# Kernel optimization log

Measured on AMD Instinct MI355X. Metric: run time of the kernel, lower is better.

## Reference

```python
import jax, jax.numpy as jnp
import numpy as np

B, N, DIN, DH = 16, 512, 128, 256
NEG = -9.0e15  # matches -9000000000000000.0 in torch source


def _xavier(key, fan_in, fan_out):
    lim = float(np.sqrt(6.0 / (fan_in + fan_out)))
    return jax.random.uniform(key, (fan_in, fan_out), jnp.float32, -lim, lim)


def _l2n(x, eps=1e-12):
    # torch F.normalize: x / max(||x||, eps)
    return x / jnp.maximum(jnp.linalg.norm(x, axis=-1, keepdims=True), eps)


def _prelu(x, a):
    return jnp.where(x >= 0, x, a * x)


def setup_inputs() -> dict:
    key = jax.random.key(0)
    ks = jax.random.split(key, 12)
    seq = jax.random.normal(ks[0], (B, N, DIN), jnp.float32)
    # sparse-ish nonnegative adjacency with self loops, row-normalized
    u = jax.random.uniform(ks[1], (B, N, N), jnp.float32)
    a = jnp.where(u < 0.1, u, 0.0) + jnp.eye(N, dtype=jnp.float32)[None]
    adj = a / a.sum(-1, keepdims=True)
    # dense diffusion matrix, row-normalized
    d = jax.random.uniform(ks[2], (B, N, N), jnp.float32)
    diff = d / d.sum(-1, keepdims=True)
    # dropout keep-mask for F.dropout(p=0.1, training=True)
    keep = jax.random.bernoulli(ks[3], 0.9, (B, N, N)).astype(jnp.float32)
    drop_mask = keep / 0.9
    return {
        "seq": seq, "adj": adj, "diff": diff, "drop_mask": drop_mask,
        "fc1_w": _xavier(ks[4], DIN, DH),
        "q_w": _xavier(ks[5], DH, DH),
        "k_w": _xavier(ks[6], DH, DH),
        "v_w1": _xavier(ks[7], DH, DH),
        "v_w2": _xavier(ks[8], DH, DH),
        "fc2_w": _xavier(ks[9], DIN, DH),
        "bias1": jnp.zeros((DH,), jnp.float32),
        "bias2": jnp.zeros((DH,), jnp.float32),
        "prelu1_a": jnp.float32(0.25),
        "prelu2_a": jnp.float32(0.25),
        "v_prelu_a": jnp.float32(0.25),
    }


def reference(seq, adj, diff, drop_mask, fc1_w, q_w, k_w, v_w1, v_w2,
              fc2_w, bias1, bias2, prelu1_a, prelu2_a, v_prelu_a):
    # ---- GCN1 (attention branch) ----
    fts = seq @ fc1_w                                   # [B,N,H]
    out = jnp.einsum('bmn,bnh->bmh', adj, fts)          # adj aggregation
    q = _l2n(out @ q_w)
    k = _l2n(out @ k_w)
    scores = jax.lax.stop_gradient(jnp.einsum('bmd,bnd->bmn', q, k))  # .detach()
    div_loss = jnp.mean(jnp.sum((q - k) ** 2, axis=-1))
    att = jnp.where(adj > 0, scores, NEG)
    att = jax.nn.softmax(att, axis=-1) * drop_mask      # dropout(p=0.1)
    agg = jnp.einsum('bmn,bnh->bmh', att, out)
    v = _prelu(agg @ v_w1, v_prelu_a) @ v_w2 + bias1
    h1 = _prelu(v, prelu1_a)
    # ---- GCN2 (plain branch) ----
    h2 = _prelu(jnp.einsum('bmn,bnh->bmh', diff, seq @ fc2_w) + bias2, prelu2_a)
    # ---- Readout ----
    c1 = jnp.mean(h1, axis=1)                           # [B,H]
    c2 = jnp.mean(h2, axis=1)
    # ---- DIS ----
    n1 = _l2n(h1).reshape(B * N, DH)
    n2 = _l2n(h2).reshape(B * N, DH)
    node_logits = n1 @ n2.T                             # [B*N, B*N]
    graph_logits = _l2n(c1) @ _l2n(c2).T                # [B, B]
    return node_logits, graph_logits, div_loss
```

## Files before the change

### kernel.cpp

```cpp
#include <hip/hip_runtime.h>
#include <hip/hip_bf16.h>


using bf16x8 = __attribute__((ext_vector_type(8))) short;
using f32x4  = __attribute__((ext_vector_type(4))) float;

__device__ __forceinline__ unsigned short f2b(float f) {
    union { float f; unsigned int u; } x; x.f = f;
    unsigned int r = x.u + 0x7FFFu + ((x.u >> 16) & 1u);
    return (unsigned short)(r >> 16);
}
__device__ __forceinline__ void gload_lds16(const void* g, void* l) {
    __builtin_amdgcn_global_load_lds(
        (const __attribute__((address_space(1))) void*)g,
        (__attribute__((address_space(3))) void*)l, 16, 0, 0);
}

__global__ __launch_bounds__(256) void prep(
    const float* __restrict__ seq, const float* __restrict__ adj,
    const float* __restrict__ diff,
    const float* __restrict__ fc1, const float* __restrict__ fc2,
    const float* __restrict__ qw,  const float* __restrict__ kw,
    const float* __restrict__ v1,  const float* __restrict__ v2,
    unsigned short* __restrict__ seq_bf, unsigned short* __restrict__ adj_bf,
    unsigned short* __restrict__ diff_bf,
    unsigned short* fc1T, unsigned short* fc2T, unsigned short* qwT,
    unsigned short* kwT,  unsigned short* v1T,  unsigned short* v2T)
{
    __shared__ float t[32][33];
    const int bid = blockIdx.x, tid = threadIdx.x;
    if (bid < 9216) {
        long i = (long)bid * 256 + tid;
        const float* src; unsigned short* dst; long off;
        if (i < 262144)       { src = seq;  dst = seq_bf;  off = i; }
        else if (i < 1310720) { src = adj;  dst = adj_bf;  off = i - 262144; }
        else                  { src = diff; dst = diff_bf; off = i - 1310720; }
        float4 v = reinterpret_cast<const float4*>(src)[off];
        ushort4 o; o.x = f2b(v.x); o.y = f2b(v.y); o.z = f2b(v.z); o.w = f2b(v.w);
        reinterpret_cast<ushort4*>(dst)[off] = o;
        return;
    }
    const int r = bid - 9216;
    const int z = r >> 6;
    const float* in; unsigned short* op; int R;
    if      (z == 0) { in = fc1; op = fc1T; R = 128; }
    else if (z == 1) { in = fc2; op = fc2T; R = 128; }
    else if (z == 2) { in = qw;  op = qwT;  R = 256; }
    else if (z == 3) { in = kw;  op = kwT;  R = 256; }
    else if (z == 4) { in = v1;  op = v1T;  R = 256; }
    else             { in = v2;  op = v2T;  R = 256; }
    const int c0 = (r & 7) * 32, r0 = ((r >> 3) & 7) * 32;
    if (r0 >= R) return;
    const int x = tid & 31, y = tid >> 5;
    for (int i = 0; i < 32; i += 8) t[y + i][x] = in[(long)(r0 + y + i) * 256 + c0 + x];
    __syncthreads();
    for (int i = 0; i < 32; i += 8)
        op[(long)(c0 + y + i) * R + r0 + x] = f2b(t[x][y + i]);
}

#define BN 128
#define BK 64

template<int TBM, bool WF, bool WB, bool SWZ>
__global__ __launch_bounds__(256) void gemm_nt(
    const unsigned short* __restrict__ A, const unsigned short* __restrict__ Bt,
    float* __restrict__ Cf, unsigned short* __restrict__ Cb,
    int M, int Nn, int K, int lda, int ldb, int ldc,
    long sA, long sB, long sC)
{
    constexpr int MI = TBM / 32;
    __shared__ unsigned short As[TBM][BK];
    __shared__ unsigned short Bs[BN][BK];
    const int b = blockIdx.z;
    A  += (long)b * sA;
    Bt += (long)b * sB;
    const long cbase = (long)b * sC;

    int tx, ty;
    if (SWZ) {
        int bid = blockIdx.y * gridDim.x + blockIdx.x;
        int nwg = gridDim.x * gridDim.y;
        int cpx = nwg >> 3;
        int s = (bid & 7) * cpx + (bid >> 3);
        tx = s % gridDim.x; ty = s / gridDim.x;
    } else { tx = blockIdx.x; ty = blockIdx.y; }
    const int tile_m = ty * TBM;
    const int tile_n = tx * BN;

    const int tid  = threadIdx.x;
    const int lane = tid & 63;
    const int wave = tid >> 6;
    const int wm = (wave >> 1) * (TBM / 2);
    const int wn = (wave & 1) << 6;
    const int lrow = lane >> 3;
    const int lcol = (lane & 7) << 3;

    f32x4 acc[MI][4] = {};

    for (int k0 = 0; k0 < K; k0 += BK) {
        #pragma unroll
        for (int i = 0; i < TBM / 32; ++i) {
            const int rb = (i * 4 + wave) * 8;
            gload_lds16(A + (long)(tile_m + rb + lrow) * lda + k0 + lcol, &As[rb][0]);
        }
        #pragma unroll
        for (int i = 0; i < 4; ++i) {
            const int rb = (i * 4 + wave) * 8;
            gload_lds16(Bt + (long)(tile_n + rb + lrow) * ldb + k0 + lcol, &Bs[rb][0]);
        }
        __syncthreads();
        #pragma unroll
        for (int ks = 0; ks < 2; ++ks) {
            const int kk = ks * 32 + ((lane >> 4) << 3);
            bf16x8 af[MI], bq[4];
            #pragma unroll
            for (int mi = 0; mi < MI; ++mi)
                af[mi] = *reinterpret_cast<const bf16x8*>(&As[wm + (lane & 15) + mi * 16][kk]);
            #pragma unroll
            for (int ni = 0; ni < 4; ++ni)
                bq[ni] = *reinterpret_cast<const bf16x8*>(&Bs[wn + (lane & 15) + ni * 16][kk]);
            #pragma unroll
            for (int mi = 0; mi < MI; ++mi)
                #pragma unroll
                for (int ni = 0; ni < 4; ++ni)
                    acc[mi][ni] = __builtin_amdgcn_mfma_f32_16x16x32_bf16(
                        af[mi], bq[ni], acc[mi][ni], 0, 0, 0);
        }
        __syncthreads();
    }

    const int c0 = lane & 15;
    const int r0 = (lane >> 4) << 2;
    #pragma unroll
    for (int ni = 0; ni < 4; ++ni) {
        const int col = tile_n + wn + ni * 16 + c0;
        #pragma unroll
        for (int mi = 0; mi < MI; ++mi) {
            const int row0 = tile_m + wm + mi * 16 + r0;
            if (WF) {
                #pragma unroll
                for (int j = 0; j < 4; ++j)
                    __builtin_nontemporal_store(acc[mi][ni][j],
                        &Cf[cbase + (long)(row0 + j) * ldc + col]);
            }
            if (WB) {
                #pragma unroll
                for (int j = 0; j < 4; ++j)
                    Cb[cbase + (long)(row0 + j) * ldc + col] = f2b(acc[mi][ni][j]);
            }
        }
    }
}

__global__ __launch_bounds__(256) void gcn1qk(
    const unsigned short* __restrict__ adj_bf,
    const unsigned short* __restrict__ ftsT,
    const unsigned short* __restrict__ qkT,
    unsigned short* __restrict__ outT,
    unsigned short* __restrict__ q_bf,
    unsigned short* __restrict__ k_bf)
{
    __shared__ unsigned char smem[86528];
    unsigned short* Ot  = (unsigned short*)smem;
    unsigned short* As  = (unsigned short*)(smem + 16896);
    unsigned short* Bs  = (unsigned short*)(smem + 20992);
    unsigned short* Bs2 = (unsigned short*)(smem + 20992);
    __shared__ float sred[32][4];

    const int b  = blockIdx.y;
    const int m0 = blockIdx.x << 5;
    const unsigned short* ap = adj_bf + ((long)b * 512 + m0) * 512;

    const int tid = threadIdx.x, lane = tid & 63, wave = tid >> 6;
    const int lrow = lane >> 3, lcol = (lane & 7) << 3;
    const int hi = lane >> 4, c0 = lane & 15, r0 = hi << 2;

    {
        const int wn = wave << 6;
        f32x4 acc[2][4] = {};
        for (int k0 = 0; k0 < 512; k0 += 64) {
            gload_lds16(ap + (long)(wave * 8 + lrow) * 512 + k0 + lcol, &As[wave * 8 * 64]);
            #pragma unroll
            for (int i = 0; i < 8; ++i) {
                const int rb = (i * 4 + wave) * 8;
                gload_lds16(ftsT + (long)(rb + lrow) * 8192 + b * 512 + k0 + lcol, &Bs[rb * 64]);
            }
            __syncthreads();
            #pragma unroll
            for (int ks = 0; ks < 2; ++ks) {
                const int kk = ks * 32 + (hi << 3);
                bf16x8 af[2], bq[4];
                #pragma unroll
                for (int mi = 0; mi < 2; ++mi)
                    af[mi] = *reinterpret_cast<const bf16x8*>(&As[(mi * 16 + c0) * 64 + kk]);
                #pragma unroll
                for (int ni = 0; ni < 4; ++ni)
                    bq[ni] = *reinterpret_cast<const bf16x8*>(&Bs[(wn + ni * 16 + c0) * 64 + kk]);
                #pragma unroll
                for (int mi = 0; mi < 2; ++mi)
                    #pragma unroll
                    for (int ni = 0; ni < 4; ++ni)
                        acc[mi][ni] = __builtin_amdgcn_mfma_f32_16x16x32_bf16(
                            af[mi], bq[ni], acc[mi][ni], 0, 0, 0);
            }
            __syncthreads();
        }
        #pragma unroll
        for (int mi = 0; mi < 2; ++mi)
            #pragma unroll
            for (int ni = 0; ni < 4; ++ni) {
                const int col = wn + ni * 16 + c0;
                ushort4 o;
                unsigned short* e = (unsigned short*)&o;
                #pragma unroll
                for (int j = 0; j < 4; ++j) {
                    unsigned short v = f2b(acc[mi][ni][j]);
                    e[j] = v;
                    Ot[(mi * 16 + r0 + j) * 264 + col] = v;
                }
                *reinterpret_cast<ushort4*>(
                    &outT[(long)b * 131072 + (long)col * 512 + m0 + mi * 16 + r0]) = o;
            }
    }
    __syncthreads();

    {
        const int wn = wave << 7;
        f32x4 acc[2][8] = {};
        for (int k0 = 0; k0 < 256; k0 += 64) {
            #pragma unroll
            for (int i = 0; i < 16; ++i) {
                const int rb = (i * 4 + wave) * 8;
                gload_lds16(qkT + (long)(rb + lrow) * 256 + k0 + lcol, &Bs2[rb * 64]);
            }
            __syncthreads();
            #pragma unroll
            for (int ks = 0; ks < 2; ++ks) {
                const int kk = ks * 32 + (hi << 3);
                bf16x8 af[2], bq[8];
                #pragma unroll
                for (int mi = 0; mi < 2; ++mi)
                    af[mi] = *reinterpret_cast<const bf16x8*>(&Ot[(mi * 16 + c0) * 264 + k0 + kk]);
                #pragma unroll
                for (int ni = 0; ni < 8; ++ni)
                    bq[ni] = *reinterpret_cast<const bf16x8*>(&Bs2[(wn + ni * 16 + c0) * 64 + kk]);
                #pragma unroll
                for (int mi = 0; mi < 2; ++mi)
                    #pragma unroll
                    for (int ni = 0; ni < 8; ++ni)
                        acc[mi][ni] = __builtin_amdgcn_mfma_f32_16x16x32_bf16(
                            af[mi], bq[ni], acc[mi][ni], 0, 0, 0);
            }
            __syncthreads();
        }
        float rs[2][4] = {};
        #pragma unroll
        for (int mi = 0; mi < 2; ++mi)
            #pragma unroll
            for (int ni = 0; ni < 8; ++ni)
                #pragma unroll
                for (int j = 0; j < 4; ++j) { float x = acc[mi][ni][j]; rs[mi][j] += x * x; }
        #pragma unroll
        for (int o = 1; o <= 8; o <<= 1)
            #pragma unroll
            for (int mi = 0; mi < 2; ++mi)
                #pragma unroll
                for (int j = 0; j < 4; ++j) rs[mi][j] += __shfl_xor(rs[mi][j], o);
        if (c0 == 0) {
            #pragma unroll
            for (int mi = 0; mi < 2; ++mi)
                #pragma unroll
                for (int j = 0; j < 4; ++j) sred[mi * 16 + r0 + j][wave] = rs[mi][j];
        }
        __syncthreads();
        float inv[2][4];
        #pragma unroll
        for (int mi = 0; mi < 2; ++mi)
            #pragma unroll
            for (int j = 0; j < 4; ++j) {
                const int rr = mi * 16 + r0 + j;
                float sq = sred[rr][0] + sred[rr][1];
                float sk = sred[rr][2] + sred[rr][3];
                inv[mi][j] = 1.f / fmaxf(sqrtf(wave < 2 ? sq : sk), 1e-12f);
            }
        #pragma unroll
        for (int mi = 0; mi < 2; ++mi)
            #pragma unroll
            for (int ni = 0; ni < 8; ++ni)
                #pragma unroll
                for (int j = 0; j < 4; ++j) {
                    const long rowg = (long)b * 512 + m0 + mi * 16 + r0 + j;
                    const int col = wn + ni * 16 + c0;
                    unsigned short v = f2b(acc[mi][ni][j] * inv[mi][j]);
                    if (wave < 2) q_bf[rowg * 256 + col] = v;
                    else          k_bf[rowg * 256 + col - 256] = v;
                }
    }
}

__global__ __launch_bounds__(256) void attmlp(
    const unsigned short* __restrict__ q_bf,
    const unsigned short* __restrict__ k_bf,
    const unsigned short* __restrict__ adj_bf,
    const float* __restrict__ drop,
    const unsigned short* __restrict__ outT,
    const unsigned short* __restrict__ w1T,
    const unsigned short* __restrict__ w2T,
    const float* __restrict__ bias,
    const float* __restrict__ av, const float* __restrict__ a1,
    unsigned short* __restrict__ n_out,
    float* __restrict__ psum,
    float* __restrict__ rowpart)
{
    __shared__ unsigned char smem[69632];
    unsigned short* As  = (unsigned short*)smem;
    unsigned short* Bs  = (unsigned short*)(smem + 4096);
    unsigned short* Pls = (unsigned short*)smem;
    unsigned short* Bs2 = (unsigned short*)(smem + 34816);
    unsigned short* T   = (unsigned short*)smem;
    unsigned short* Bs3 = (unsigned short*)(smem + 16896);
    __shared__ float redm[32][4], reds[32][4];

    const int b  = blockIdx.y;
    const int m0 = blockIdx.x << 5;
    const unsigned short* qp = q_bf + (long)b * 131072 + (long)m0 * 256;
    const unsigned short* kp = k_bf + (long)b * 131072;
    const unsigned short* ot = outT + (long)b * 131072;
    const unsigned short* ap = adj_bf + ((long)b * 512 + m0) * 512;
    const float*          dp = drop   + ((long)b * 512 + m0) * 512;

    const int tid = threadIdx.x, lane = tid & 63, wave = tid >> 6;
    const int lrow = lane >> 3, lcol = (lane & 7) << 3;
    const int hi = lane >> 4, c0 = lane & 15, r0 = hi << 2;

    {
        const int wn = wave << 7;
        f32x4 acc[2][8] = {};
        for (int k0 = 0; k0 < 256; k0 += 64) {
            gload_lds16(qp + (long)(wave * 8 + lrow) * 256 + k0 + lcol, &As[wave * 8 * 64]);
            #pragma unroll
            for (int i = 0; i < 16; ++i) {
                const int rb = (i * 4 + wave) * 8;
                gload_lds16(kp + (long)(rb + lrow) * 256 + k0 + lcol, &Bs[rb * 64]);
            }
            __syncthreads();
            #pragma unroll
            for (int ks = 0; ks < 2; ++ks) {
                const int kk = ks * 32 + (hi << 3);
                bf16x8 af[2], bq[8];
                #pragma unroll
                for (int mi = 0; mi < 2; ++mi)
                    af[mi] = *reinterpret_cast<const bf16x8*>(&As[(mi * 16 + c0) * 64 + kk]);
                #pragma unroll
                for (int ni = 0; ni < 8; ++ni)
                    bq[ni] = *reinterpret_cast<const bf16x8*>(&Bs[(wn + ni * 16 + c0) * 64 + kk]);
                #pragma unroll
                for (int mi = 0; mi < 2; ++mi)
                    #pragma unroll
                    for (int ni = 0; ni < 8; ++ni)
                        acc[mi][ni] = __builtin_amdgcn_mfma_f32_16x16x32_bf16(
                            af[mi], bq[ni], acc[mi][ni], 0, 0, 0);
            }
            __syncthreads();
        }

        float rmax[2][4];
        #pragma unroll
        for (int mi = 0; mi < 2; ++mi)
            #pragma unroll
            for (int j = 0; j < 4; ++j) rmax[mi][j] = -3.0e38f;
        #pragma unroll
        for (int mi = 0; mi < 2; ++mi)
            #pragma unroll
            for (int ni = 0; ni < 8; ++ni)
                #pragma unroll
                for (int j = 0; j < 4; ++j) {
                    const int rowl = mi * 16 + r0 + j;
                    const int col  = wn + ni * 16 + c0;
                    float s = acc[mi][ni][j];
                    if (col == m0 + rowl)
                        rowpart[(long)b * 512 + m0 + rowl] = 2.f - 2.f * s;
                    bool m = ap[(long)rowl * 512 + col] != 0;
                    s = m ? s : -3.0e38f;
                    acc[mi][ni][j] = s;
                    rmax[mi][j] = fmaxf(rmax[mi][j], s);
                }
        #pragma unroll
        for (int o = 1; o <= 8; o <<= 1)
            #pragma unroll
            for (int mi = 0; mi < 2; ++mi)
                #pragma unroll
                for (int j = 0; j < 4; ++j)
                    rmax[mi][j] = fmaxf(rmax[mi][j], __shfl_xor(rmax[mi][j], o));
        if (c0 == 0) {
            #pragma unroll
            for (int mi = 0; mi < 2; ++mi)
                #pragma unroll
                for (int j = 0; j < 4; ++j) redm[mi * 16 + r0 + j][wave] = rmax[mi][j];
        }
        __syncthreads();
        float mx[2][4], rsum[2][4];
        #pragma unroll
        for (int mi = 0; mi < 2; ++mi)
            #pragma unroll
            for (int j = 0; j < 4; ++j) {
                const int rr = mi * 16 + r0 + j;
                mx[mi][j] = fmaxf(fmaxf(redm[rr][0], redm[rr][1]), fmaxf(redm[rr][2], redm[rr][3]));
                rsum[mi][j] = 0.f;
            }
        #pragma unroll
        for (int mi = 0; mi < 2; ++mi)
            #pragma unroll
            for (int ni = 0; ni < 8; ++ni)
                #pragma unroll
                for (int j = 0; j < 4; ++j) {
                    float e = __expf(acc[mi][ni][j] - mx[mi][j]);
                    acc[mi][ni][j] = e;
                    rsum[mi][j] += e;
                }
        #pragma unroll
        for (int o = 1; o <= 8; o <<= 1)
            #pragma unroll
            for (int mi = 0; mi < 2; ++mi)
                #pragma unroll
                for (int j = 0; j < 4; ++j) rsum[mi][j] += __shfl_xor(rsum[mi][j], o);
        if (c0 == 0) {
            #pragma unroll
            for (int mi = 0; mi < 2; ++mi)
                #pragma unroll
                for (int j = 0; j < 4; ++j) reds[mi * 16 + r0 + j][wave] = rsum[mi][j];
        }
        __syncthreads();
        float inv[2][4];
        #pragma unroll
        for (int mi = 0; mi < 2; ++mi)
            #pragma unroll
            for (int j = 0; j < 4; ++j) {
                const int rr = mi * 16 + r0 + j;
                inv[mi][j] = 1.f / (reds[rr][0] + reds[rr][1] + reds[rr][2] + reds[rr][3]);
            }
        #pragma unroll
        for (int mi = 0; mi < 2; ++mi)
            #pragma unroll
            for (int ni = 0; ni < 8; ++ni)
                #pragma unroll
                for (int j = 0; j < 4; ++j) {
                    const int rowl = mi * 16 + r0 + j;
                    const int col  = wn + ni * 16 + c0;
                    float p = acc[mi][ni][j] * inv[mi][j] * dp[(long)rowl * 512 + col];
                    Pls[rowl * 520 + col] = f2b(p);
                }
    }
    __syncthreads();

    f32x4 acc2[2][4] = {};
    {
        const int wn = wave << 6;
        for (int k0 = 0; k0 < 512; k0 += 64) {
            #pragma unroll
            for (int i = 0; i < 8; ++i) {
                const int rb = (i * 4 + wave) * 8;
                gload_lds16(ot + (long)(rb + lrow) * 512 + k0 + lcol, &Bs2[rb * 64]);
            }
            __syncthreads();
            #pragma unroll
            for (int ks = 0; ks < 2; ++ks) {
                const int kk = ks * 32 + (hi << 3);
                bf16x8 af[2], bq[4];
                #pragma unroll
                for (int mi = 0; mi < 2; ++mi)
                    af[mi] = *reinterpret_cast<const bf16x8*>(&Pls[(mi * 16 + c0) * 520 + k0 + kk]);
                #pragma unroll
                for (int ni = 0; ni < 4; ++ni)
                    bq[ni] = *reinterpret_cast<const bf16x8*>(&Bs2[(wn + ni * 16 + c0) * 64 + kk]);
                #pragma unroll
                for (int mi = 0; mi < 2; ++mi)
                    #pragma unroll
                    for (int ni = 0; ni < 4; ++ni)
                        acc2[mi][ni] = __builtin_amdgcn_mfma_f32_16x16x32_bf16(
                            af[mi], bq[ni], acc2[mi][ni], 0, 0, 0);
            }
            __syncthreads();
        }
    }

    const int wn6 = wave << 6;
    const float alphav = av[0];
    #pragma unroll
    for (int mi = 0; mi < 2; ++mi)
        #pragma unroll
        for (int ni = 0; ni < 4; ++ni)
            #pragma unroll
            for (int j = 0; j < 4; ++j)
                T[(mi * 16 + r0 + j) * 264 + wn6 + ni * 16 + c0] = f2b(acc2[mi][ni][j]);
    f32x4 acct[2][4] = {};
    for (int k0 = 0; k0 < 256; k0 += 64) {
        #pragma unroll
        for (int i = 0; i < 8; ++i) {
            const int rb = (i * 4 + wave) * 8;
            gload_lds16(w1T + (long)(rb + lrow) * 256 + k0 + lcol, &Bs3[rb * 64]);
        }
        __syncthreads();
        #pragma unroll
        for (int ks = 0; ks < 2; ++ks) {
            const int kk = ks * 32 + (hi << 3);
            bf16x8 af[2], bq[4];
            #pragma unroll
            for (int mi = 0; mi < 2; ++mi)
                af[mi] = *reinterpret_cast<const bf16x8*>(&T[(mi * 16 + c0) * 264 + k0 + kk]);
            #pragma unroll
            for (int ni = 0; ni < 4; ++ni)
                bq[ni] = *reinterpret_cast<const bf16x8*>(&Bs3[(wn6 + ni * 16 + c0) * 64 + kk]);
            #pragma unroll
            for (int mi = 0; mi < 2; ++mi)
                #pragma unroll
                for (int ni = 0; ni < 4; ++ni)
                    acct[mi][ni] = __builtin_amdgcn_mfma_f32_16x16x32_bf16(
                        af[mi], bq[ni], acct[mi][ni], 0, 0, 0);
        }
        __syncthreads();
    }
    #pragma unroll
    for (int mi = 0; mi < 2; ++mi)
        #pragma unroll
        for (int ni = 0; ni < 4; ++ni)
            #pragma unroll
            for (int j = 0; j < 4; ++j) {
                float x = acct[mi][ni][j];
                x = (x >= 0.f) ? x : alphav * x;
                T[(mi * 16 + r0 + j) * 264 + wn6 + ni * 16 + c0] = f2b(x);
            }

    f32x4 acc3[2][4] = {};
    for (int k0 = 0; k0 < 256; k0 += 64) {
        #pragma unroll
        for (int i = 0; i < 8; ++i) {
            const int rb = (i * 4 + wave) * 8;
            gload_lds16(w2T + (long)(rb + lrow) * 256 + k0 + lcol, &Bs3[rb * 64]);
        }
        __syncthreads();
        #pragma unroll
        for (int ks = 0; ks < 2; ++ks) {
            const int kk = ks * 32 + (hi << 3);
            bf16x8 af[2], bq[4];
            #pragma unroll
            for (int mi = 0; mi < 2; ++mi)
                af[mi] = *reinterpret_cast<const bf16x8*>(&T[(mi * 16 + c0) * 264 + k0 + kk]);
            #pragma unroll
            for (int ni = 0; ni < 4; ++ni)
                bq[ni] = *reinterpret_cast<const bf16x8*>(&Bs3[(wn6 + ni * 16 + c0) * 64 + kk]);
            #pragma unroll
            for (int mi = 0; mi < 2; ++mi)
                #pragma unroll
                for (int ni = 0; ni < 4; ++ni)
                    acc3[mi][ni] = __builtin_amdgcn_mfma_f32_16x16x32_bf16(
                        af[mi], bq[ni], acc3[mi][ni], 0, 0, 0);
        }
        __syncthreads();
    }

    const float alpha1 = a1[0];
    float rs[2][4] = {};
    #pragma unroll
    for (int ni = 0; ni < 4; ++ni) {
        const float bv = bias[wn6 + ni * 16 + c0];
        #pragma unroll
        for (int mi = 0; mi < 2; ++mi)
            #pragma unroll
            for (int j = 0; j < 4; ++j) {
                float x = acc3[mi][ni][j] + bv;
                x = (x >= 0.f) ? x : alpha1 * x;
                acc3[mi][ni][j] = x;
                rs[mi][j] += x * x;
            }
    }
    #pragma unroll
    for (int o = 1; o <= 8; o <<= 1)
        #pragma unroll
        for (int mi = 0; mi < 2; ++mi)
            #pragma unroll
            for (int j = 0; j < 4; ++j) rs[mi][j] += __shfl_xor(rs[mi][j], o);
    if (c0 == 0) {
        #pragma unroll
        for (int mi = 0; mi < 2; ++mi)
            #pragma unroll
            for (int j = 0; j < 4; ++j) redm[mi * 16 + r0 + j][wave] = rs[mi][j];
    }
    __syncthreads();
    float inv2[2][4];
    #pragma unroll
    for (int mi = 0; mi < 2; ++mi)
        #pragma unroll
        for (int j = 0; j < 4; ++j) {
            const int rr = mi * 16 + r0 + j;
            float s = redm[rr][0] + redm[rr][1] + redm[rr][2] + redm[rr][3];
            inv2[mi][j] = 1.f / fmaxf(sqrtf(s), 1e-12f);
        }
    float cs[4];
    #pragma unroll
    for (int ni = 0; ni < 4; ++ni) {
        float s = 0.f;
        #pragma unroll
        for (int mi = 0; mi < 2; ++mi)
            #pragma unroll
            for (int j = 0; j < 4; ++j) s += acc3[mi][ni][j];
        s += __shfl_xor(s, 16);
        s += __shfl_xor(s, 32);
        cs[ni] = s;
    }
    const int p = b * 16 + blockIdx.x;
    if (lane < 16) {
        #pragma unroll
        for (int ni = 0; ni < 4; ++ni)
            psum[(long)p * 256 + wn6 + ni * 16 + lane] = cs[ni];
    }
    const long row0g = (long)b * 512 + m0;
    #pragma unroll
    for (int mi = 0; mi < 2; ++mi)
        #pragma unroll
        for (int ni = 0; ni < 4; ++ni)
            #pragma unroll
            for (int j = 0; j < 4; ++j)
                n_out[(row0g + mi * 16 + r0 + j) * 256 + wn6 + ni * 16 + c0] =
                    f2b(acc3[mi][ni][j] * inv2[mi][j]);
}

__global__ __launch_bounds__(256) void gemm_norm(
    const unsigned short* __restrict__ A, const unsigned short* __restrict__ Bt,
    unsigned short* __restrict__ n_out, float* __restrict__ psum,
    const float* __restrict__ bias, const float* __restrict__ alpha_ptr,
    int K, int lda, int ldb, long sA, long sB)
{
    __shared__ unsigned short As[32][BK];
    __shared__ unsigned short Bs[256][BK];
    __shared__ float rowred[32][4];
    A  += (long)blockIdx.z * sA;
    Bt += (long)blockIdx.z * sB;
    const int p = blockIdx.z * gridDim.y + blockIdx.y;
    const int arow0 = blockIdx.y * 32;
    const long grow0 = (long)p * 32;

    const int tid  = threadIdx.x;
    const int lane = tid & 63;
    const int wave = tid >> 6;
    const int wn = wave << 6;
    const int lrow = lane >> 3;
    const int lcol = (lane & 7) << 3;

    f32x4 acc[2][4] = {};

    for (int k0 = 0; k0 < K; k0 += BK) {
        {
            const int rb = wave * 8;
            gload_lds16(A + (long)(arow0 + rb + lrow) * lda + k0 + lcol, &As[rb][0]);
        }
        #pragma unroll
        for (int i = 0; i < 8; ++i) {
            const int rb = (i * 4 + wave) * 8;
            gload_lds16(Bt + (long)(rb + lrow) * ldb + k0 + lcol, &Bs[rb][0]);
        }
        __syncthreads();
        #pragma unroll
        for (int ks = 0; ks < 2; ++ks) {
            const int kk = ks * 32 + ((lane >> 4) << 3);
            bf16x8 af[2], bq[4];
            #pragma unroll
            for (int mi = 0; mi < 2; ++mi)
                af[mi] = *reinterpret_cast<const bf16x8*>(&As[(lane & 15) + mi * 16][kk]);
            #pragma unroll
            for (int ni = 0; ni < 4; ++ni)
                bq[ni] = *reinterpret_cast<const bf16x8*>(&Bs[wn + (lane & 15) + ni * 16][kk]);
            #pragma unroll
            for (int mi = 0; mi < 2; ++mi)
                #pragma unroll
                for (int ni = 0; ni < 4; ++ni)
                    acc[mi][ni] = __builtin_amdgcn_mfma_f32_16x16x32_bf16(
                        af[mi], bq[ni], acc[mi][ni], 0, 0, 0);
        }
        __syncthreads();
    }

    const float alpha = alpha_ptr[0];
    const int c0 = lane & 15;
    const int r0 = (lane >> 4) << 2;
    float rs[2][4] = {};
    #pragma unroll
    for (int ni = 0; ni < 4; ++ni) {
        const float bv = bias[wn + ni * 16 + c0];
        #pragma unroll
        for (int mi = 0; mi < 2; ++mi)
            #pragma unroll
            for (int j = 0; j < 4; ++j) {
                float x = acc[mi][ni][j] + bv;
                x = (x >= 0.f) ? x : alpha * x;
                acc[mi][ni][j] = x;
                rs[mi][j] += x * x;
            }
    }
    #pragma unroll
    for (int o = 1; o <= 8; o <<= 1)
        #pragma unroll
        for (int mi = 0; mi < 2; ++mi)
            #pragma unroll
            for (int j = 0; j < 4; ++j) rs[mi][j] += __shfl_xor(rs[mi][j], o);
    if ((lane & 15) == 0) {
        #pragma unroll
        for (int mi = 0; mi < 2; ++mi)
            #pragma unroll
            for (int j = 0; j < 4; ++j) rowred[mi * 16 + r0 + j][wave] = rs[mi][j];
    }
    __syncthreads();
    float inv[2][4];
    #pragma unroll
    for (int mi = 0; mi < 2; ++mi)
        #pragma unroll
        for (int j = 0; j < 4; ++j) {
            const int r = mi * 16 + r0 + j;
            float s = rowred[r][0] + rowred[r][1] + rowred[r][2] + rowred[r][3];
            inv[mi][j] = 1.f / fmaxf(sqrtf(s), 1e-12f);
        }
    float cs[4];
    #pragma unroll
    for (int ni = 0; ni < 4; ++ni) {
        float s = 0.f;
        #pragma unroll
        for (int mi = 0; mi < 2; ++mi)
            #pragma unroll
            for (int j = 0; j < 4; ++j) s += acc[mi][ni][j];
        s += __shfl_xor(s, 16);
        s += __shfl_xor(s, 32);
        cs[ni] = s;
    }
    if (lane < 16) {
        #pragma unroll
        for (int ni = 0; ni < 4; ++ni)
            psum[(long)p * 256 + wn + ni * 16 + lane] = cs[ni];
    }
    #pragma unroll
    for (int ni = 0; ni < 4; ++ni)
        #pragma unroll
        for (int mi = 0; mi < 2; ++mi)
            #pragma unroll
            for (int j = 0; j < 4; ++j)
                n_out[(grow0 + mi * 16 + r0 + j) * 256 + wn + ni * 16 + c0] =
                    f2b(acc[mi][ni][j] * inv[mi][j]);
}

__global__ __launch_bounds__(256) void creduce(const float* __restrict__ psum1,
                                               const float* __restrict__ psum2,
                                               float* __restrict__ c1n,
                                               float* __restrict__ c2n) {
    const int which = blockIdx.x & 1, g = blockIdx.x >> 1;
    const float* ps = which ? psum2 : psum1;
    float* cn = which ? c2n : c1n;
    const int t = threadIdx.x;
    float s = 0.f;
    #pragma unroll
    for (int c = 0; c < 16; ++c) s += ps[(long)(g * 16 + c) * 256 + t];
    s *= (1.f / 512.f);
    float ss = s * s;
    #pragma unroll
    for (int o = 32; o; o >>= 1) ss += __shfl_xor(ss, o);
    __shared__ float red[4];
    if ((t & 63) == 0) red[t >> 6] = ss;
    __syncthreads();
    float tot = red[0] + red[1] + red[2] + red[3];
    cn[g * 256 + t] = s / fmaxf(sqrtf(tot), 1e-12f);
}

__global__ __launch_bounds__(256) void graphf3(const float* __restrict__ c1n,
                                               const float* __restrict__ c2n,
                                               const float* __restrict__ rowpart,
                                               float* __restrict__ out_g,
                                               float* __restrict__ out_div) {
    const int t = threadIdx.x, ii = t >> 4, jj = t & 15;
    float s = 0.f;
    for (int h = 0; h < 256; ++h) s += c1n[ii * 256 + h] * c2n[jj * 256 + h];
    out_g[ii * 16 + jj] = s;
    float ds = 0.f;
    for (int i = t; i < 8192; i += 256) ds += rowpart[i];
    #pragma unroll
    for (int o = 32; o; o >>= 1) ds += __shfl_xor(ds, o);
    __shared__ float red[4];
    if ((t & 63) == 0) red[t >> 6] = ds;
    __syncthreads();
    if (t == 0) out_div[0] = (red[0] + red[1] + red[2] + red[3]) * (1.f / 8192.f);
}

static constexpr long OFF_SEQ_BF  = 0;
static constexpr long OFF_FC1T    = 2097152;
static constexpr long OFF_QWT     = 2228224;
static constexpr long OFF_VW1T    = 2490368;
static constexpr long OFF_VW2T    = 2621440;
static constexpr long OFF_ADJ     = 3145728;
static constexpr long OFF_DIFF    = 11534336;
static constexpr long OFF_FTST    = 19922944;
static constexpr long OFF_OUTT    = 28311552;
static constexpr long OFF_QBF     = 32505856;
static constexpr long OFF_KBF     = 36700160;
static constexpr long OFF_N1      = 40894464;
static constexpr long OFF_N2      = 45088768;
static constexpr long OFF_PSUM    = 49283072;
static constexpr long OFF_ROWPART = 49807360;
static constexpr long OFF_C1N     = 49840128;
static constexpr long OFF_C2N     = 49856512;

extern "C" void kernel_launch(void* const* d_in, const int* in_sizes, int n_in,
                              void* d_out, int out_size, void* d_ws, size_t ws_size,
                              hipStream_t stream) {
    const float* seq      = (const float*)d_in[0];
    const float* adj      = (const float*)d_in[1];
    const float* diff     = (const float*)d_in[2];
    const float* drop     = (const float*)d_in[3];
    const float* fc1_w    = (const float*)d_in[4];
    const float* q_w      = (const float*)d_in[5];
    const float* k_w      = (const float*)d_in[6];
    const float* v_w1     = (const float*)d_in[7];
    const float* v_w2     = (const float*)d_in[8];
    const float* fc2_w    = (const float*)d_in[9];
    const float* bias1    = (const float*)d_in[10];
    const float* bias2    = (const float*)d_in[11];
    const float* prelu1_a = (const float*)d_in[12];
    const float* prelu2_a = (const float*)d_in[13];
    const float* v_prelu  = (const float*)d_in[14];
    float* out = (float*)d_out;

    char* ws = (char*)d_ws;
    unsigned short* seq_bf  = (unsigned short*)(ws + OFF_SEQ_BF);
    unsigned short* fc1T    = (unsigned short*)(ws + OFF_FC1T);
    unsigned short* fc2T    = (unsigned short*)(ws + OFF_FC1T + 65536);
    unsigned short* qwT     = (unsigned short*)(ws + OFF_QWT);
    unsigned short* kwT     = (unsigned short*)(ws + OFF_QWT + 131072);
    unsigned short* vw1T    = (unsigned short*)(ws + OFF_VW1T);
    unsigned short* vw2T    = (unsigned short*)(ws + OFF_VW2T);
    unsigned short* adj_bf  = (unsigned short*)(ws + OFF_ADJ);
    unsigned short* diff_bf = (unsigned short*)(ws + OFF_DIFF);
    unsigned short* ftsT    = (unsigned short*)(ws + OFF_FTST);
    unsigned short* fts2T   = (unsigned short*)(ws + OFF_FTST + 4194304);
    unsigned short* outT    = (unsigned short*)(ws + OFF_OUTT);
    unsigned short* q_bf    = (unsigned short*)(ws + OFF_QBF);
    unsigned short* k_bf    = (unsigned short*)(ws + OFF_KBF);
    unsigned short* n1_bf   = (unsigned short*)(ws + OFF_N1);
    unsigned short* n2_bf   = (unsigned short*)(ws + OFF_N2);
    float*          psum1   = (float*)(ws + OFF_PSUM);
    float*          psum2   = (float*)(ws + OFF_PSUM + 262144);
    float*          rowpart = (float*)(ws + OFF_ROWPART);
    float*          c1n     = (float*)(ws + OFF_C1N);
    float*          c2n     = (float*)(ws + OFF_C2N);

    prep<<<9600, 256, 0, stream>>>(seq, adj, diff, fc1_w, fc2_w, q_w, k_w, v_w1, v_w2,
                                   seq_bf, adj_bf, diff_bf, fc1T, fc2T, qwT, kwT, vw1T, vw2T);

    gemm_nt<64, false, true, false><<<dim3(64, 4, 2), 256, 0, stream>>>(
        fc1T, seq_bf, nullptr, ftsT,
        256, 8192, 128, 128, 128, 8192, 32768, 0, 2097152);

    gcn1qk<<<dim3(16, 16), 256, 0, stream>>>(adj_bf, ftsT, qwT, outT, q_bf, k_bf);

    gemm_norm<<<dim3(1, 16, 16), 256, 0, stream>>>(
        diff_bf, fts2T, n2_bf, psum2, bias2, prelu2_a, 512, 512, 8192, 262144, 512);

    attmlp<<<dim3(16, 16), 256, 0, stream>>>(
        q_bf, k_bf, adj_bf, drop, outT, vw1T, vw2T, bias1, v_prelu, prelu1_a,
        n1_bf, psum1, rowpart);

    creduce<<<32, 256, 0, stream>>>(psum1, psum2, c1n, c2n);
    graphf3<<<1, 256, 0, stream>>>(c1n, c2n, rowpart, out + 67108864, out + 67109120);

    gemm_nt<128, true, false, true><<<dim3(64, 64, 1), 256, 0, stream>>>(
        n1_bf, n2_bf, out, nullptr,
        8192, 8192, 256, 256, 256, 8192, 0, 0, 0);

    (void)in_sizes; (void)n_in; (void)out_size; (void)ws_size;
}
```

Measured before the change: 212.5 us.

## Halve gcn1qk row tile and merge GCN2 norm kernel into attention kernel

gcn1qk now processes 16 rows per block instead of 32, doubling the grid to 512 blocks and shrinking shared memory so more blocks can run per CU. The separate GCN2 gemm_norm launch is folded into the attention/MLP kernel: odd blocks run the attention path and even blocks run the diffusion GEMM with bias, PReLU and normalization, so the two independent branches share one launch and fill the device together. The large node-logits store also switches from nontemporal to regular stores. The trade-offs are lower MFMA reuse per block in gcn1qk and possible load imbalance between the two block types in the merged kernel.

```diff
diff --git a/kernel.cpp b/kernel.cpp
--- a/kernel.cpp
+++ b/kernel.cpp
@@ -140,8 +140,7 @@
             if (WF) {
                 #pragma unroll
                 for (int j = 0; j < 4; ++j)
-                    __builtin_nontemporal_store(acc[mi][ni][j],
-                        &Cf[cbase + (long)(row0 + j) * ldc + col]);
+                    Cf[cbase + (long)(row0 + j) * ldc + col] = acc[mi][ni][j];
             }
             if (WB) {
                 #pragma unroll
@@ -160,15 +159,15 @@
     unsigned short* __restrict__ q_bf,
     unsigned short* __restrict__ k_bf)
 {
-    __shared__ unsigned char smem[86528];
+    __shared__ unsigned char smem[73984];
     unsigned short* Ot  = (unsigned short*)smem;
-    unsigned short* As  = (unsigned short*)(smem + 16896);
-    unsigned short* Bs  = (unsigned short*)(smem + 20992);
-    unsigned short* Bs2 = (unsigned short*)(smem + 20992);
-    __shared__ float sred[32][4];
+    unsigned short* As  = (unsigned short*)(smem + 8448);
+    unsigned short* Bs  = (unsigned short*)(smem + 10496);
+    unsigned short* Bs2 = (unsigned short*)(smem + 8448);
+    __shared__ float sred[16][4];
 
     const int b  = blockIdx.y;
-    const int m0 = blockIdx.x << 5;
+    const int m0 = blockIdx.x << 4;
     const unsigned short* ap = adj_bf + ((long)b * 512 + m0) * 512;
 
     const int tid = threadIdx.x, lane = tid & 63, wave = tid >> 6;
@@ -177,9 +176,10 @@
 
     {
         const int wn = wave << 6;
-        f32x4 acc[2][4] = {};
+        f32x4 acc[4] = {};
         for (int k0 = 0; k0 < 512; k0 += 64) {
-            gload_lds16(ap + (long)(wave * 8 + lrow) * 512 + k0 + lcol, &As[wave * 8 * 64]);
+            if (wave < 2)
+                gload_lds16(ap + (long)(wave * 8 + lrow) * 512 + k0 + lcol, &As[wave * 8 * 64]);
             #pragma unroll
             for (int i = 0; i < 8; ++i) {
                 const int rb = (i * 4 + wave) * 8;
@@ -189,44 +189,34 @@
             #pragma unroll
             for (int ks = 0; ks < 2; ++ks) {
                 const int kk = ks * 32 + (hi << 3);
-                bf16x8 af[2], bq[4];
-                #pragma unroll
-                for (int mi = 0; mi < 2; ++mi)
-                    af[mi] = *reinterpret_cast<const bf16x8*>(&As[(mi * 16 + c0) * 64 + kk]);
-                #pragma unroll
-                for (int ni = 0; ni < 4; ++ni)
-                    bq[ni] = *reinterpret_cast<const bf16x8*>(&Bs[(wn + ni * 16 + c0) * 64 + kk]);
-                #pragma unroll
-                for (int mi = 0; mi < 2; ++mi)
-                    #pragma unroll
-                    for (int ni = 0; ni < 4; ++ni)
-                        acc[mi][ni] = __builtin_amdgcn_mfma_f32_16x16x32_bf16(
-                            af[mi], bq[ni], acc[mi][ni], 0, 0, 0);
-            }
-            __syncthreads();
-        }
-        #pragma unroll
-        for (int mi = 0; mi < 2; ++mi)
-            #pragma unroll
-            for (int ni = 0; ni < 4; ++ni) {
-                const int col = wn + ni * 16 + c0;
-                ushort4 o;
-                unsigned short* e = (unsigned short*)&o;
-                #pragma unroll
-                for (int j = 0; j < 4; ++j) {
-                    unsigned short v = f2b(acc[mi][ni][j]);
-                    e[j] = v;
-                    Ot[(mi * 16 + r0 + j) * 264 + col] = v;
-                }
-                *reinterpret_cast<ushort4*>(
-                    &outT[(long)b * 131072 + (long)col * 512 + m0 + mi * 16 + r0]) = o;
-            }
+                bf16x8 af = *reinterpret_cast<const bf16x8*>(&As[c0 * 64 + kk]);
+                #pragma unroll
+                for (int ni = 0; ni < 4; ++ni) {
+                    bf16x8 bq = *reinterpret_cast<const bf16x8*>(&Bs[(wn + ni * 16 + c0) * 64 + kk]);
+                    acc[ni] = __builtin_amdgcn_mfma_f32_16x16x32_bf16(af, bq, acc[ni], 0, 0, 0);
+                }
+            }
+            __syncthreads();
+        }
+        #pragma unroll
+        for (int ni = 0; ni < 4; ++ni) {
+            const int col = wn + ni * 16 + c0;
+            ushort4 o;
+            unsigned short* e = (unsigned short*)&o;
+            #pragma unroll
+            for (int j = 0; j < 4; ++j) {
+                unsigned short v = f2b(acc[ni][j]);
+                e[j] = v;
+                Ot[(r0 + j) * 264 + col] = v;
+            }
+            *reinterpret_cast<ushort4*>(
+                &outT[(long)b * 131072 + (long)col * 512 + m0 + r0]) = o;
+        }
     }
-    __syncthreads();
 
     {
         const int wn = wave << 7;
-        f32x4 acc[2][8] = {};
+        f32x4 acc[8] = {};
         for (int k0 = 0; k0 < 256; k0 += 64) {
             #pragma unroll
             for (int i = 0; i < 16; ++i) {
@@ -237,68 +227,51 @@
             #pragma unroll
             for (int ks = 0; ks < 2; ++ks) {
                 const int kk = ks * 32 + (hi << 3);
-                bf16x8 af[2], bq[8];
-                #pragma unroll
-                for (int mi = 0; mi < 2; ++mi)
-                    af[mi] = *reinterpret_cast<const bf16x8*>(&Ot[(mi * 16 + c0) * 264 + k0 + kk]);
-                #pragma unroll
-                for (int ni = 0; ni < 8; ++ni)
-                    bq[ni] = *reinterpret_cast<const bf16x8*>(&Bs2[(wn + ni * 16 + c0) * 64 + kk]);
-                #pragma unroll
-                for (int mi = 0; mi < 2; ++mi)
-                    #pragma unroll
-                    for (int ni = 0; ni < 8; ++ni)
-                        acc[mi][ni] = __builtin_amdgcn_mfma_f32_16x16x32_bf16(
-                            af[mi], bq[ni], acc[mi][ni], 0, 0, 0);
-            }
-            __syncthreads();
-        }
-        float rs[2][4] = {};
-        #pragma unroll
-        for (int mi = 0; mi < 2; ++mi)
-            #pragma unroll
-            for (int ni = 0; ni < 8; ++ni)
-                #pragma unroll
-                for (int j = 0; j < 4; ++j) { float x = acc[mi][ni][j]; rs[mi][j] += x * x; }
+                bf16x8 af = *reinterpret_cast<const bf16x8*>(&Ot[c0 * 264 + k0 + kk]);
+                #pragma unroll
+                for (int ni = 0; ni < 8; ++ni) {
+                    bf16x8 bq = *reinterpret_cast<const bf16x8*>(&Bs2[(wn + ni * 16 + c0) * 64 + kk]);
+                    acc[ni] = __builtin_amdgcn_mfma_f32_16x16x32_bf16(af, bq, acc[ni], 0, 0, 0);
+                }
+            }
+            __syncthreads();
+        }
+        float rs[4] = {};
+        #pragma unroll
+        for (int ni = 0; ni < 8; ++ni)
+            #pragma unroll
+            for (int j = 0; j < 4; ++j) { float x = acc[ni][j]; rs[j] += x * x; }
         #pragma unroll
         for (int o = 1; o <= 8; o <<= 1)
             #pragma unroll
-            for (int mi = 0; mi < 2; ++mi)
-                #pragma unroll
-                for (int j = 0; j < 4; ++j) rs[mi][j] += __shfl_xor(rs[mi][j], o);
+            for (int j = 0; j < 4; ++j) rs[j] += __shfl_xor(rs[j], o);
         if (c0 == 0) {
             #pragma unroll
-            for (int mi = 0; mi < 2; ++mi)
-                #pragma unroll
-                for (int j = 0; j < 4; ++j) sred[mi * 16 + r0 + j][wave] = rs[mi][j];
+            for (int j = 0; j < 4; ++j) sred[r0 + j][wave] = rs[j];
         }
         __syncthreads();
-        float inv[2][4];
-        #pragma unroll
-        for (int mi = 0; mi < 2; ++mi)
+        float inv[4];
+        #pragma unroll
+        for (int j = 0; j < 4; ++j) {
+            const int rr = r0 + j;
+            float sq = sred[rr][0] + sred[rr][1];
+            float sk = sred[rr][2] + sred[rr][3];
+            inv[j] = 1.f / fmaxf(sqrtf(wave < 2 ? sq : sk), 1e-12f);
+        }
+        #pragma unroll
+        for (int ni = 0; ni < 8; ++ni)
             #pragma unroll
             for (int j = 0; j < 4; ++j) {
-                const int rr = mi * 16 + r0 + j;
-                float sq = sred[rr][0] + sred[rr][1];
-                float sk = sred[rr][2] + sred[rr][3];
-                inv[mi][j] = 1.f / fmaxf(sqrtf(wave < 2 ? sq : sk), 1e-12f);
-            }
-        #pragma unroll
-        for (int mi = 0; mi < 2; ++mi)
-            #pragma unroll
-            for (int ni = 0; ni < 8; ++ni)
-                #pragma unroll
-                for (int j = 0; j < 4; ++j) {
-                    const long rowg = (long)b * 512 + m0 + mi * 16 + r0 + j;
-                    const int col = wn + ni * 16 + c0;
-                    unsigned short v = f2b(acc[mi][ni][j] * inv[mi][j]);
-                    if (wave < 2) q_bf[rowg * 256 + col] = v;
-                    else          k_bf[rowg * 256 + col - 256] = v;
-                }
+                const long rowg = (long)b * 512 + m0 + r0 + j;
+                const int col = wn + ni * 16 + c0;
+                unsigned short v = f2b(acc[ni][j] * inv[j]);
+                if (wave < 2) q_bf[rowg * 256 + col] = v;
+                else          k_bf[rowg * 256 + col - 256] = v;
+            }
     }
 }
 
-__global__ __launch_bounds__(256) void attmlp(
+__global__ __launch_bounds__(256) void attmlp_h2(
     const unsigned short* __restrict__ q_bf,
     const unsigned short* __restrict__ k_bf,
     const unsigned short* __restrict__ adj_bf,
@@ -306,161 +279,208 @@
     const unsigned short* __restrict__ outT,
     const unsigned short* __restrict__ w1T,
     const unsigned short* __restrict__ w2T,
-    const float* __restrict__ bias,
+    const float* __restrict__ bias1,
     const float* __restrict__ av, const float* __restrict__ a1,
-    unsigned short* __restrict__ n_out,
-    float* __restrict__ psum,
-    float* __restrict__ rowpart)
+    unsigned short* __restrict__ n1,
+    float* __restrict__ psum1,
+    float* __restrict__ rowpart,
+    const unsigned short* __restrict__ diff_bf,
+    const unsigned short* __restrict__ fts2T,
+    const float* __restrict__ bias2, const float* __restrict__ a2,
+    unsigned short* __restrict__ n2,
+    float* __restrict__ psum2)
 {
     __shared__ unsigned char smem[69632];
-    unsigned short* As  = (unsigned short*)smem;
-    unsigned short* Bs  = (unsigned short*)(smem + 4096);
-    unsigned short* Pls = (unsigned short*)smem;
-    unsigned short* Bs2 = (unsigned short*)(smem + 34816);
-    unsigned short* T   = (unsigned short*)smem;
-    unsigned short* Bs3 = (unsigned short*)(smem + 16896);
     __shared__ float redm[32][4], reds[32][4];
 
-    const int b  = blockIdx.y;
-    const int m0 = blockIdx.x << 5;
-    const unsigned short* qp = q_bf + (long)b * 131072 + (long)m0 * 256;
-    const unsigned short* kp = k_bf + (long)b * 131072;
-    const unsigned short* ot = outT + (long)b * 131072;
-    const unsigned short* ap = adj_bf + ((long)b * 512 + m0) * 512;
-    const float*          dp = drop   + ((long)b * 512 + m0) * 512;
-
+    const int idx = blockIdx.x >> 1;
     const int tid = threadIdx.x, lane = tid & 63, wave = tid >> 6;
     const int lrow = lane >> 3, lcol = (lane & 7) << 3;
     const int hi = lane >> 4, c0 = lane & 15, r0 = hi << 2;
 
-    {
-        const int wn = wave << 7;
-        f32x4 acc[2][8] = {};
+    if (blockIdx.x & 1) {
+        unsigned short* As  = (unsigned short*)smem;
+        unsigned short* Bs  = (unsigned short*)(smem + 4096);
+        unsigned short* Pls = (unsigned short*)smem;
+        unsigned short* Bs2 = (unsigned short*)(smem + 34816);
+        unsigned short* T   = (unsigned short*)smem;
+        unsigned short* Bs3 = (unsigned short*)(smem + 16896);
+
+        const int b  = idx >> 4;
+        const int m0 = (idx & 15) << 5;
+        const unsigned short* qp = q_bf + (long)b * 131072 + (long)m0 * 256;
+        const unsigned short* kp = k_bf + (long)b * 131072;
+        const unsigned short* ot = outT + (long)b * 131072;
+        const unsigned short* ap = adj_bf + ((long)b * 512 + m0) * 512;
+        const float*          dp = drop   + ((long)b * 512 + m0) * 512;
+
+        {
+            const int wn = wave << 7;
+            f32x4 acc[2][8] = {};
+            for (int k0 = 0; k0 < 256; k0 += 64) {
+                gload_lds16(qp + (long)(wave * 8 + lrow) * 256 + k0 + lcol, &As[wave * 8 * 64]);
+                #pragma unroll
+                for (int i = 0; i < 16; ++i) {
+                    const int rb = (i * 4 + wave) * 8;
+                    gload_lds16(kp + (long)(rb + lrow) * 256 + k0 + lcol, &Bs[rb * 64]);
+                }
+                __syncthreads();
+                #pragma unroll
+                for (int ks = 0; ks < 2; ++ks) {
+                    const int kk = ks * 32 + (hi << 3);
+                    bf16x8 af[2], bq[8];
+                    #pragma unroll
+                    for (int mi = 0; mi < 2; ++mi)
+                        af[mi] = *reinterpret_cast<const bf16x8*>(&As[(mi * 16 + c0) * 64 + kk]);
+                    #pragma unroll
+                    for (int ni = 0; ni < 8; ++ni)
+                        bq[ni] = *reinterpret_cast<const bf16x8*>(&Bs[(wn + ni * 16 + c0) * 64 + kk]);
+                    #pragma unroll
+                    for (int mi = 0; mi < 2; ++mi)
+                        #pragma unroll
+                        for (int ni = 0; ni < 8; ++ni)
+                            acc[mi][ni] = __builtin_amdgcn_mfma_f32_16x16x32_bf16(
+                                af[mi], bq[ni], acc[mi][ni], 0, 0, 0);
+                }
+                __syncthreads();
+            }
+
+            float rmax[2][4];
+            #pragma unroll
+            for (int mi = 0; mi < 2; ++mi)
+                #pragma unroll
+                for (int j = 0; j < 4; ++j) rmax[mi][j] = -3.0e38f;
+            #pragma unroll
+            for (int mi = 0; mi < 2; ++mi)
+                #pragma unroll
+                for (int ni = 0; ni < 8; ++ni)
+                    #pragma unroll
+                    for (int j = 0; j < 4; ++j) {
+                        const int rowl = mi * 16 + r0 + j;
+                        const int col  = wn + ni * 16 + c0;
+                        float s = acc[mi][ni][j];
+                        if (col == m0 + rowl)
+                            rowpart[(long)b * 512 + m0 + rowl] = 2.f - 2.f * s;
+                        bool m = ap[(long)rowl * 512 + col] != 0;
+                        s = m ? s : -3.0e38f;
+                        acc[mi][ni][j] = s;
+                        rmax[mi][j] = fmaxf(rmax[mi][j], s);
+                    }
+            #pragma unroll
+            for (int o = 1; o <= 8; o <<= 1)
+                #pragma unroll
+                for (int mi = 0; mi < 2; ++mi)
+                    #pragma unroll
+                    for (int j = 0; j < 4; ++j)
+                        rmax[mi][j] = fmaxf(rmax[mi][j], __shfl_xor(rmax[mi][j], o));
+            if (c0 == 0) {
+                #pragma unroll
+                for (int mi = 0; mi < 2; ++mi)
+                    #pragma unroll
+                    for (int j = 0; j < 4; ++j) redm[mi * 16 + r0 + j][wave] = rmax[mi][j];
+            }
+            __syncthreads();
+            float mx[2][4], rsum[2][4];
+            #pragma unroll
+            for (int mi = 0; mi < 2; ++mi)
+                #pragma unroll
+                for (int j = 0; j < 4; ++j) {
+                    const int rr = mi * 16 + r0 + j;
+                    mx[mi][j] = fmaxf(fmaxf(redm[rr][0], redm[rr][1]),
+                                      fmaxf(redm[rr][2], redm[rr][3]));
+                    rsum[mi][j] = 0.f;
+                }
+            #pragma unroll
+            for (int mi = 0; mi < 2; ++mi)
+                #pragma unroll
+                for (int ni = 0; ni < 8; ++ni)
+                    #pragma unroll
+                    for (int j = 0; j < 4; ++j) {
+                        float e = __expf(acc[mi][ni][j] - mx[mi][j]);
+                        acc[mi][ni][j] = e;
+                        rsum[mi][j] += e;
+                    }
+            #pragma unroll
+            for (int o = 1; o <= 8; o <<= 1)
+                #pragma unroll
+                for (int mi = 0; mi < 2; ++mi)
+                    #pragma unroll
+                    for (int j = 0; j < 4; ++j) rsum[mi][j] += __shfl_xor(rsum[mi][j], o);
+            if (c0 == 0) {
+                #pragma unroll
+                for (int mi = 0; mi < 2; ++mi)
+                    #pragma unroll
+                    for (int j = 0; j < 4; ++j) reds[mi * 16 + r0 + j][wave] = rsum[mi][j];
+            }
+            __syncthreads();
+            float inv[2][4];
+            #pragma unroll
+            for (int mi = 0; mi < 2; ++mi)
+                #pragma unroll
+                for (int j = 0; j < 4; ++j) {
+                    const int rr = mi * 16 + r0 + j;
+                    inv[mi][j] = 1.f / (reds[rr][0] + reds[rr][1] + reds[rr][2] + reds[rr][3]);
+                }
+            #pragma unroll
+            for (int mi = 0; mi < 2; ++mi)
+                #pragma unroll
+                for (int ni = 0; ni < 8; ++ni)
+                    #pragma unroll
+                    for (int j = 0; j < 4; ++j) {
+                        const int rowl = mi * 16 + r0 + j;
+                        const int col  = wn + ni * 16 + c0;
+                        float p = acc[mi][ni][j] * inv[mi][j] * dp[(long)rowl * 512 + col];
+                        Pls[rowl * 520 + col] = f2b(p);
+                    }
+        }
+        __syncthreads();
+
+        f32x4 acc2[2][4] = {};
+        {
+            const int wn = wave << 6;
+            for (int k0 = 0; k0 < 512; k0 += 64) {
+                #pragma unroll
+                for (int i = 0; i < 8; ++i) {
+                    const int rb = (i * 4 + wave) * 8;
+                    gload_lds16(ot + (long)(rb + lrow) * 512 + k0 + lcol, &Bs2[rb * 64]);
+                }
+                __syncthreads();
+                #pragma unroll
+                for (int ks = 0; ks < 2; ++ks) {
+                    const int kk = ks * 32 + (hi << 3);
+                    bf16x8 af[2], bq[4];
+                    #pragma unroll
+                    for (int mi = 0; mi < 2; ++mi)
+                        af[mi] = *reinterpret_cast<const bf16x8*>(&Pls[(mi * 16 + c0) * 520 + k0 + kk]);
+                    #pragma unroll
+                    for (int ni = 0; ni < 4; ++ni)
+                        bq[ni] = *reinterpret_cast<const bf16x8*>(&Bs2[(wn + ni * 16 + c0) * 64 + kk]);
+                    #pragma unroll
+                    for (int mi = 0; mi < 2; ++mi)
+                        #pragma unroll
+                        for (int ni = 0; ni < 4; ++ni)
+                            acc2[mi][ni] = __builtin_amdgcn_mfma_f32_16x16x32_bf16(
+                                af[mi], bq[ni], acc2[mi][ni], 0, 0, 0);
+                }
+                __syncthreads();
+            }
+        }
+
+        const int wn6 = wave << 6;
+        const float alphav = av[0];
+        #pragma unroll
+        for (int mi = 0; mi < 2; ++mi)
+            #pragma unroll
+            for (int ni = 0; ni < 4; ++ni)
+                #pragma unroll
+                for (int j = 0; j < 4; ++j)
+                    T[(mi * 16 + r0 + j) * 264 + wn6 + ni * 16 + c0] = f2b(acc2[mi][ni][j]);
+        f32x4 acct[2][4] = {};
         for (int k0 = 0; k0 < 256; k0 += 64) {
-            gload_lds16(qp + (long)(wave * 8 + lrow) * 256 + k0 + lcol, &As[wave * 8 * 64]);
-            #pragma unroll
-            for (int i = 0; i < 16; ++i) {
-                const int rb = (i * 4 + wave) * 8;
-                gload_lds16(kp + (long)(rb + lrow) * 256 + k0 + lcol, &Bs[rb * 64]);
-            }
-            __syncthreads();
-            #pragma unroll
-            for (int ks = 0; ks < 2; ++ks) {
-                const int kk = ks * 32 + (hi << 3);
-                bf16x8 af[2], bq[8];
-                #pragma unroll
-                for (int mi = 0; mi < 2; ++mi)
-                    af[mi] = *reinterpret_cast<const bf16x8*>(&As[(mi * 16 + c0) * 64 + kk]);
-                #pragma unroll
-                for (int ni = 0; ni < 8; ++ni)
-                    bq[ni] = *reinterpret_cast<const bf16x8*>(&Bs[(wn + ni * 16 + c0) * 64 + kk]);
-                #pragma unroll
-                for (int mi = 0; mi < 2; ++mi)
-                    #pragma unroll
-                    for (int ni = 0; ni < 8; ++ni)
-                        acc[mi][ni] = __builtin_amdgcn_mfma_f32_16x16x32_bf16(
-                            af[mi], bq[ni], acc[mi][ni], 0, 0, 0);
-            }
-            __syncthreads();
-        }
-
-        float rmax[2][4];
-        #pragma unroll
-        for (int mi = 0; mi < 2; ++mi)
-            #pragma unroll
-            for (int j = 0; j < 4; ++j) rmax[mi][j] = -3.0e38f;
-        #pragma unroll
-        for (int mi = 0; mi < 2; ++mi)
-            #pragma unroll
-            for (int ni = 0; ni < 8; ++ni)
-                #pragma unroll
-                for (int j = 0; j < 4; ++j) {
-                    const int rowl = mi * 16 + r0 + j;
-                    const int col  = wn + ni * 16 + c0;
-                    float s = acc[mi][ni][j];
-                    if (col == m0 + rowl)
-                        rowpart[(long)b * 512 + m0 + rowl] = 2.f - 2.f * s;
-                    bool m = ap[(long)rowl * 512 + col] != 0;
-                    s = m ? s : -3.0e38f;
-                    acc[mi][ni][j] = s;
-                    rmax[mi][j] = fmaxf(rmax[mi][j], s);
-                }
-        #pragma unroll
-        for (int o = 1; o <= 8; o <<= 1)
-            #pragma unroll
-            for (int mi = 0; mi < 2; ++mi)
-                #pragma unroll
-                for (int j = 0; j < 4; ++j)
-                    rmax[mi][j] = fmaxf(rmax[mi][j], __shfl_xor(rmax[mi][j], o));
-        if (c0 == 0) {
-            #pragma unroll
-            for (int mi = 0; mi < 2; ++mi)
-                #pragma unroll
-                for (int j = 0; j < 4; ++j) redm[mi * 16 + r0 + j][wave] = rmax[mi][j];
-        }
-        __syncthreads();
-        float mx[2][4], rsum[2][4];
-        #pragma unroll
-        for (int mi = 0; mi < 2; ++mi)
-            #pragma unroll
-            for (int j = 0; j < 4; ++j) {
-                const int rr = mi * 16 + r0 + j;
-                mx[mi][j] = fmaxf(fmaxf(redm[rr][0], redm[rr][1]), fmaxf(redm[rr][2], redm[rr][3]));
-                rsum[mi][j] = 0.f;
-            }
-        #pragma unroll
-        for (int mi = 0; mi < 2; ++mi)
-            #pragma unroll
-            for (int ni = 0; ni < 8; ++ni)
-                #pragma unroll
-                for (int j = 0; j < 4; ++j) {
-                    float e = __expf(acc[mi][ni][j] - mx[mi][j]);
-                    acc[mi][ni][j] = e;
-                    rsum[mi][j] += e;
-                }
-        #pragma unroll
-        for (int o = 1; o <= 8; o <<= 1)
-            #pragma unroll
-            for (int mi = 0; mi < 2; ++mi)
-                #pragma unroll
-                for (int j = 0; j < 4; ++j) rsum[mi][j] += __shfl_xor(rsum[mi][j], o);
-        if (c0 == 0) {
-            #pragma unroll
-            for (int mi = 0; mi < 2; ++mi)
-                #pragma unroll
-                for (int j = 0; j < 4; ++j) reds[mi * 16 + r0 + j][wave] = rsum[mi][j];
-        }
-        __syncthreads();
-        float inv[2][4];
-        #pragma unroll
-        for (int mi = 0; mi < 2; ++mi)
-            #pragma unroll
-            for (int j = 0; j < 4; ++j) {
-                const int rr = mi * 16 + r0 + j;
-                inv[mi][j] = 1.f / (reds[rr][0] + reds[rr][1] + reds[rr][2] + reds[rr][3]);
-            }
-        #pragma unroll
-        for (int mi = 0; mi < 2; ++mi)
-            #pragma unroll
-            for (int ni = 0; ni < 8; ++ni)
-                #pragma unroll
-                for (int j = 0; j < 4; ++j) {
-                    const int rowl = mi * 16 + r0 + j;
-                    const int col  = wn + ni * 16 + c0;
-                    float p = acc[mi][ni][j] * inv[mi][j] * dp[(long)rowl * 512 + col];
-                    Pls[rowl * 520 + col] = f2b(p);
-                }
-    }
-    __syncthreads();
-
-    f32x4 acc2[2][4] = {};
-    {
-        const int wn = wave << 6;
-        for (int k0 = 0; k0 < 512; k0 += 64) {
             #pragma unroll
             for (int i = 0; i < 8; ++i) {
                 const int rb = (i * 4 + wave) * 8;
-                gload_lds16(ot + (long)(rb + lrow) * 512 + k0 + lcol, &Bs2[rb * 64]);
+                gload_lds16(w1T + (long)(rb + lrow) * 256 + k0 + lcol, &Bs3[rb * 64]);
             }
             __syncthreads();
             #pragma unroll
@@ -469,281 +489,227 @@
                 bf16x8 af[2], bq[4];
                 #pragma unroll
                 for (int mi = 0; mi < 2; ++mi)
-                    af[mi] = *reinterpret_cast<const bf16x8*>(&Pls[(mi * 16 + c0) * 520 + k0 + kk]);
+                    af[mi] = *reinterpret_cast<const bf16x8*>(&T[(mi * 16 + c0) * 264 + k0 + kk]);
                 #pragma unroll
                 for (int ni = 0; ni < 4; ++ni)
-                    bq[ni] = *reinterpret_cast<const bf16x8*>(&Bs2[(wn + ni * 16 + c0) * 64 + kk]);
+                    bq[ni] = *reinterpret_cast<const bf16x8*>(&Bs3[(wn6 + ni * 16 + c0) * 64 + kk]);
                 #pragma unroll
                 for (int mi = 0; mi < 2; ++mi)
                     #pragma unroll
                     for (int ni = 0; ni < 4; ++ni)
-                        acc2[mi][ni] = __builtin_amdgcn_mfma_f32_16x16x32_bf16(
-                            af[mi], bq[ni], acc2[mi][ni], 0, 0, 0);
-            }
-            __syncthreads();
-        }
+                        acct[mi][ni] = __builtin_amdgcn_mfma_f32_16x16x32_bf16(
+                            af[mi], bq[ni], acct[mi][ni], 0, 0, 0);
+            }
+            __syncthreads();
+        }
+        #pragma unroll
+        for (int mi = 0; mi < 2; ++mi)
+            #pragma unroll
+            for (int ni = 0; ni < 4; ++ni)
+                #pragma unroll
+                for (int j = 0; j < 4; ++j) {
+                    float x = acct[mi][ni][j];
+                    x = (x >= 0.f) ? x : alphav * x;
+                    T[(mi * 16 + r0 + j) * 264 + wn6 + ni * 16 + c0] = f2b(x);
+                }
+
+        f32x4 acc3[2][4] = {};
+        for (int k0 = 0; k0 < 256; k0 += 64) {
+            #pragma unroll
+            for (int i = 0; i < 8; ++i) {
+                const int rb = (i * 4 + wave) * 8;
+                gload_lds16(w2T + (long)(rb + lrow) * 256 + k0 + lcol, &Bs3[rb * 64]);
+            }
+            __syncthreads();
+            #pragma unroll
+            for (int ks = 0; ks < 2; ++ks) {
+                const int kk = ks * 32 + (hi << 3);
+                bf16x8 af[2], bq[4];
+                #pragma unroll
+                for (int mi = 0; mi < 2; ++mi)
+                    af[mi] = *reinterpret_cast<const bf16x8*>(&T[(mi * 16 + c0) * 264 + k0 + kk]);
+                #pragma unroll
+                for (int ni = 0; ni < 4; ++ni)
+                    bq[ni] = *reinterpret_cast<const bf16x8*>(&Bs3[(wn6 + ni * 16 + c0) * 64 + kk]);
+                #pragma unroll
+                for (int mi = 0; mi < 2; ++mi)
+                    #pragma unroll
+                    for (int ni = 0; ni < 4; ++ni)
+                        acc3[mi][ni] = __builtin_amdgcn_mfma_f32_16x16x32_bf16(
+                            af[mi], bq[ni], acc3[mi][ni], 0, 0, 0);
+            }
+            __syncthreads();
+        }
+
+        const float alpha1 = a1[0];
+        float rs[2][4] = {};
+        #pragma unroll
+        for (int ni = 0; ni < 4; ++ni) {
+            const float bv = bias1[wn6 + ni * 16 + c0];
+            #pragma unroll
+            for (int mi = 0; mi < 2; ++mi)
+                #pragma unroll
+                for (int j = 0; j < 4; ++j) {
+                    float x = acc3[mi][ni][j] + bv;
+                    x = (x >= 0.f) ? x : alpha1 * x;
+                    acc3[mi][ni][j] = x;
+                    rs[mi][j] += x * x;
+                }
+        }
+        #pragma unroll
+        for (int o = 1; o <= 8; o <<= 1)
+            #pragma unroll
+            for (int mi = 0; mi < 2; ++mi)
+                #pragma unroll
+                for (int j = 0; j < 4; ++j) rs[mi][j] += __shfl_xor(rs[mi][j], o);
+        if (c0 == 0) {
+            #pragma unroll
+            for (int mi = 0; mi < 2; ++mi)
+                #pragma unroll
+                for (int j = 0; j < 4; ++j) redm[mi * 16 + r0 + j][wave] = rs[mi][j];
+        }
+        __syncthreads();
+        float inv2[2][4];
+        #pragma unroll
+        for (int mi = 0; mi < 2; ++mi)
+            #pragma unroll
+            for (int j = 0; j < 4; ++j) {
+                const int rr = mi * 16 + r0 + j;
+                float s = redm[rr][0] + redm[rr][1] + redm[rr][2] + redm[rr][3];
+                inv2[mi][j] = 1.f / fmaxf(sqrtf(s), 1e-12f);
+            }
+        float cs[4];
+        #pragma unroll
+        for (int ni = 0; ni < 4; ++ni) {
+            float s = 0.f;
+            #pragma unroll
+            for (int mi = 0; mi < 2; ++mi)
+                #pragma unroll
+                for (int j = 0; j < 4; ++j) s += acc3[mi][ni][j];
+            s += __shfl_xor(s, 16);
+            s += __shfl_xor(s, 32);
+            cs[ni] = s;
+        }
+        if (lane < 16) {
+            #pragma unroll
+            for (int ni = 0; ni < 4; ++ni)
+                psum1[(long)idx * 256 + wn6 + ni * 16 + lane] = cs[ni];
+        }
+        const long row0g = (long)b * 512 + m0;
+        #pragma unroll
+        for (int mi = 0; mi < 2; ++mi)
+            #pragma unroll
+            for (int ni = 0; ni < 4; ++ni)
+                #pragma unroll
+                for (int j = 0; j < 4; ++j)
+                    n1[(row0g + mi * 16 + r0 + j) * 256 + wn6 + ni * 16 + c0] =
+                        f2b(acc3[mi][ni][j] * inv2[mi][j]);
+    } else {
+        unsigned short* As = (unsigned short*)smem;
+        unsigned short* Bs = (unsigned short*)(smem + 4096);
+
+        const int z = idx >> 4;
+        const int arow0 = (idx & 15) << 5;
+        const unsigned short* A = diff_bf + (long)z * 262144;
+        const unsigned short* Bt = fts2T + z * 512;
+        const int wn = wave << 6;
+
+        f32x4 acc[2][4] = {};
+        for (int k0 = 0; k0 < 512; k0 += 64) {
+            {
+                const int rb = wave * 8;
+                gload_lds16(A + (long)(arow0 + rb + lrow) * 512 + k0 + lcol, &As[rb * 64]);
+            }
+            #pragma unroll
+            for (int i = 0; i < 8; ++i) {
+                const int rb = (i * 4 + wave) * 8;
+                gload_lds16(Bt + (long)(rb + lrow) * 8192 + k0 + lcol, &Bs[rb * 64]);
+            }
+            __syncthreads();
+            #pragma unroll
+            for (int ks = 0; ks < 2; ++ks) {
+                const int kk = ks * 32 + (hi << 3);
+                bf16x8 af[2], bq[4];
+                #pragma unroll
+                for (int mi = 0; mi < 2; ++mi)
+                    af[mi] = *reinterpret_cast<const bf16x8*>(&As[(mi * 16 + c0) * 64 + kk]);
+                #pragma unroll
+                for (int ni = 0; ni < 4; ++ni)
+                    bq[ni] = *reinterpret_cast<const bf16x8*>(&Bs[(wn + ni * 16 + c0) * 64 + kk]);
+                #pragma unroll
+                for (int mi = 0; mi < 2; ++mi)
+                    #pragma unroll
+                    for (int ni = 0; ni < 4; ++ni)
+                        acc[mi][ni] = __builtin_amdgcn_mfma_f32_16x16x32_bf16(
+                            af[mi], bq[ni], acc[mi][ni], 0, 0, 0);
+            }
+            __syncthreads();
+        }
+
+        const float alpha = a2[0];
+        float rs[2][4] = {};
+        #pragma unroll
+        for (int ni = 0; ni < 4; ++ni) {
+            const float bv = bias2[wn + ni * 16 + c0];
+            #pragma unroll
+            for (int mi = 0; mi < 2; ++mi)
+                #pragma unroll
+                for (int j = 0; j < 4; ++j) {
+                    float x = acc[mi][ni][j] + bv;
+                    x = (x >= 0.f) ? x : alpha * x;
+                    acc[mi][ni][j] = x;
+                    rs[mi][j] += x * x;
+                }
+        }
+        #pragma unroll
+        for (int o = 1; o <= 8; o <<= 1)
+            #pragma unroll
+            for (int mi = 0; mi < 2; ++mi)
+                #pragma unroll
+                for (int j = 0; j < 4; ++j) rs[mi][j] += __shfl_xor(rs[mi][j], o);
+        if (c0 == 0) {
+            #pragma unroll
+            for (int mi = 0; mi < 2; ++mi)
+                #pragma unroll
+                for (int j = 0; j < 4; ++j) redm[mi * 16 + r0 + j][wave] = rs[mi][j];
+        }
+        __syncthreads();
+        float inv[2][4];
+        #pragma unroll
+        for (int mi = 0; mi < 2; ++mi)
+            #pragma unroll
+            for (int j = 0; j < 4; ++j) {
+                const int rr = mi * 16 + r0 + j;
+                float s = redm[rr][0] + redm[rr][1] + redm[rr][2] + redm[rr][3];
+                inv[mi][j] = 1.f / fmaxf(sqrtf(s), 1e-12f);
+            }
+        float cs[4];
+        #pragma unroll
+        for (int ni = 0; ni < 4; ++ni) {
+            float s = 0.f;
+            #pragma unroll
+            for (int mi = 0; mi < 2; ++mi)
+                #pragma unroll
+                for (int j = 0; j < 4; ++j) s += acc[mi][ni][j];
+            s += __shfl_xor(s, 16);
+            s += __shfl_xor(s, 32);
+            cs[ni] = s;
+        }
+        if (lane < 16) {
+            #pragma unroll
+            for (int ni = 0; ni < 4; ++ni)
+                psum2[(long)idx * 256 + wn + ni * 16 + lane] = cs[ni];
+        }
+        const long grow0 = (long)idx * 32;
+        #pragma unroll
+        for (int mi = 0; mi < 2; ++mi)
+            #pragma unroll
+            for (int ni = 0; ni < 4; ++ni)
+                #pragma unroll
+                for (int j = 0; j < 4; ++j)
+                    n2[(grow0 + mi * 16 + r0 + j) * 256 + wn + ni * 16 + c0] =
+                        f2b(acc[mi][ni][j] * inv[mi][j]);
     }
-
-    const int wn6 = wave << 6;
-    const float alphav = av[0];
-    #pragma unroll
-    for (int mi = 0; mi < 2; ++mi)
-        #pragma unroll
-        for (int ni = 0; ni < 4; ++ni)
-            #pragma unroll
-            for (int j = 0; j < 4; ++j)
-                T[(mi * 16 + r0 + j) * 264 + wn6 + ni * 16 + c0] = f2b(acc2[mi][ni][j]);
-    f32x4 acct[2][4] = {};
-    for (int k0 = 0; k0 < 256; k0 += 64) {
-        #pragma unroll
-        for (int i = 0; i < 8; ++i) {
-            const int rb = (i * 4 + wave) * 8;
-            gload_lds16(w1T + (long)(rb + lrow) * 256 + k0 + lcol, &Bs3[rb * 64]);
-        }
-        __syncthreads();
-        #pragma unroll
-        for (int ks = 0; ks < 2; ++ks) {
-            const int kk = ks * 32 + (hi << 3);
-            bf16x8 af[2], bq[4];
-            #pragma unroll
-            for (int mi = 0; mi < 2; ++mi)
-                af[mi] = *reinterpret_cast<const bf16x8*>(&T[(mi * 16 + c0) * 264 + k0 + kk]);
-            #pragma unroll
-            for (int ni = 0; ni < 4; ++ni)
-                bq[ni] = *reinterpret_cast<const bf16x8*>(&Bs3[(wn6 + ni * 16 + c0) * 64 + kk]);
-            #pragma unroll
-            for (int mi = 0; mi < 2; ++mi)
-                #pragma unroll
-                for (int ni = 0; ni < 4; ++ni)
-                    acct[mi][ni] = __builtin_amdgcn_mfma_f32_16x16x32_bf16(
-                        af[mi], bq[ni], acct[mi][ni], 0, 0, 0);
-        }
-        __syncthreads();
-    }
-    #pragma unroll
-    for (int mi = 0; mi < 2; ++mi)
-        #pragma unroll
-        for (int ni = 0; ni < 4; ++ni)
-            #pragma unroll
-            for (int j = 0; j < 4; ++j) {
-                float x = acct[mi][ni][j];
-                x = (x >= 0.f) ? x : alphav * x;
-                T[(mi * 16 + r0 + j) * 264 + wn6 + ni * 16 + c0] = f2b(x);
-            }
-
-    f32x4 acc3[2][4] = {};
-    for (int k0 = 0; k0 < 256; k0 += 64) {
-        #pragma unroll
-        for (int i = 0; i < 8; ++i) {
-            const int rb = (i * 4 + wave) * 8;
-            gload_lds16(w2T + (long)(rb + lrow) * 256 + k0 + lcol, &Bs3[rb * 64]);
-        }
-        __syncthreads();
-        #pragma unroll
-        for (int ks = 0; ks < 2; ++ks) {
-            const int kk = ks * 32 + (hi << 3);
-            bf16x8 af[2], bq[4];
-            #pragma unroll
-            for (int mi = 0; mi < 2; ++mi)
-                af[mi] = *reinterpret_cast<const bf16x8*>(&T[(mi * 16 + c0) * 264 + k0 + kk]);
-            #pragma unroll
-            for (int ni = 0; ni < 4; ++ni)
-                bq[ni] = *reinterpret_cast<const bf16x8*>(&Bs3[(wn6 + ni * 16 + c0) * 64 + kk]);
-            #pragma unroll
-            for (int mi = 0; mi < 2; ++mi)
-                #pragma unroll
-                for (int ni = 0; ni < 4; ++ni)
-                    acc3[mi][ni] = __builtin_amdgcn_mfma_f32_16x16x32_bf16(
-                        af[mi], bq[ni], acc3[mi][ni], 0, 0, 0);
-        }
-        __syncthreads();
-    }
-
-    const float alpha1 = a1[0];
-    float rs[2][4] = {};
-    #pragma unroll
-    for (int ni = 0; ni < 4; ++ni) {
-        const float bv = bias[wn6 + ni * 16 + c0];
-        #pragma unroll
-        for (int mi = 0; mi < 2; ++mi)
-            #pragma unroll
-            for (int j = 0; j < 4; ++j) {
-                float x = acc3[mi][ni][j] + bv;
-                x = (x >= 0.f) ? x : alpha1 * x;
-                acc3[mi][ni][j] = x;
-                rs[mi][j] += x * x;
-            }
-    }
-    #pragma unroll
-    for (int o = 1; o <= 8; o <<= 1)
-        #pragma unroll
-        for (int mi = 0; mi < 2; ++mi)
-            #pragma unroll
-            for (int j = 0; j < 4; ++j) rs[mi][j] += __shfl_xor(rs[mi][j], o);
-    if (c0 == 0) {
-        #pragma unroll
-        for (int mi = 0; mi < 2; ++mi)
-            #pragma unroll
-            for (int j = 0; j < 4; ++j) redm[mi * 16 + r0 + j][wave] = rs[mi][j];
-    }
-    __syncthreads();
-    float inv2[2][4];
-    #pragma unroll
-    for (int mi = 0; mi < 2; ++mi)
-        #pragma unroll
-        for (int j = 0; j < 4; ++j) {
-            const int rr = mi * 16 + r0 + j;
-            float s = redm[rr][0] + redm[rr][1] + redm[rr][2] + redm[rr][3];
-            inv2[mi][j] = 1.f / fmaxf(sqrtf(s), 1e-12f);
-        }
-    float cs[4];
-    #pragma unroll
-    for (int ni = 0; ni < 4; ++ni) {
-        float s = 0.f;
-        #pragma unroll
-        for (int mi = 0; mi < 2; ++mi)
-            #pragma unroll
-            for (int j = 0; j < 4; ++j) s += acc3[mi][ni][j];
-        s += __shfl_xor(s, 16);
-        s += __shfl_xor(s, 32);
-        cs[ni] = s;
-    }
-    const int p = b * 16 + blockIdx.x;
-    if (lane < 16) {
-        #pragma unroll
-        for (int ni = 0; ni < 4; ++ni)
-            psum[(long)p * 256 + wn6 + ni * 16 + lane] = cs[ni];
-    }
-    const long row0g = (long)b * 512 + m0;
-    #pragma unroll
-    for (int mi = 0; mi < 2; ++mi)
-        #pragma unroll
-        for (int ni = 0; ni < 4; ++ni)
-            #pragma unroll
-            for (int j = 0; j < 4; ++j)
-                n_out[(row0g + mi * 16 + r0 + j) * 256 + wn6 + ni * 16 + c0] =
-                    f2b(acc3[mi][ni][j] * inv2[mi][j]);
-}
-
-__global__ __launch_bounds__(256) void gemm_norm(
-    const unsigned short* __restrict__ A, const unsigned short* __restrict__ Bt,
-    unsigned short* __restrict__ n_out, float* __restrict__ psum,
-    const float* __restrict__ bias, const float* __restrict__ alpha_ptr,
-    int K, int lda, int ldb, long sA, long sB)
-{
-    __shared__ unsigned short As[32][BK];
-    __shared__ unsigned short Bs[256][BK];
-    __shared__ float rowred[32][4];
-    A  += (long)blockIdx.z * sA;
-    Bt += (long)blockIdx.z * sB;
-    const int p = blockIdx.z * gridDim.y + blockIdx.y;
-    const int arow0 = blockIdx.y * 32;
-    const long grow0 = (long)p * 32;
-
-    const int tid  = threadIdx.x;
-    const int lane = tid & 63;
-    const int wave = tid >> 6;
-    const int wn = wave << 6;
-    const int lrow = lane >> 3;
-    const int lcol = (lane & 7) << 3;
-
-    f32x4 acc[2][4] = {};
-
-    for (int k0 = 0; k0 < K; k0 += BK) {
-        {
-            const int rb = wave * 8;
-            gload_lds16(A + (long)(arow0 + rb + lrow) * lda + k0 + lcol, &As[rb][0]);
-        }
-        #pragma unroll
-        for (int i = 0; i < 8; ++i) {
-            const int rb = (i * 4 + wave) * 8;
-            gload_lds16(Bt + (long)(rb + lrow) * ldb + k0 + lcol, &Bs[rb][0]);
-        }
-        __syncthreads();
-        #pragma unroll
-        for (int ks = 0; ks < 2; ++ks) {
-            const int kk = ks * 32 + ((lane >> 4) << 3);
-            bf16x8 af[2], bq[4];
-            #pragma unroll
-            for (int mi = 0; mi < 2; ++mi)
-                af[mi] = *reinterpret_cast<const bf16x8*>(&As[(lane & 15) + mi * 16][kk]);
-            #pragma unroll
-            for (int ni = 0; ni < 4; ++ni)
-                bq[ni] = *reinterpret_cast<const bf16x8*>(&Bs[wn + (lane & 15) + ni * 16][kk]);
-            #pragma unroll
-            for (int mi = 0; mi < 2; ++mi)
-                #pragma unroll
-                for (int ni = 0; ni < 4; ++ni)
-                    acc[mi][ni] = __builtin_amdgcn_mfma_f32_16x16x32_bf16(
-                        af[mi], bq[ni], acc[mi][ni], 0, 0, 0);
-        }
-        __syncthreads();
-    }
-
-    const float alpha = alpha_ptr[0];
-    const int c0 = lane & 15;
-    const int r0 = (lane >> 4) << 2;
-    float rs[2][4] = {};
-    #pragma unroll
-    for (int ni = 0; ni < 4; ++ni) {
-        const float bv = bias[wn + ni * 16 + c0];
-        #pragma unroll
-        for (int mi = 0; mi < 2; ++mi)
-            #pragma unroll
-            for (int j = 0; j < 4; ++j) {
-                float x = acc[mi][ni][j] + bv;
-                x = (x >= 0.f) ? x : alpha * x;
-                acc[mi][ni][j] = x;
-                rs[mi][j] += x * x;
-            }
-    }
-    #pragma unroll
-    for (int o = 1; o <= 8; o <<= 1)
-        #pragma unroll
-        for (int mi = 0; mi < 2; ++mi)
-            #pragma unroll
-            for (int j = 0; j < 4; ++j) rs[mi][j] += __shfl_xor(rs[mi][j], o);
-    if ((lane & 15) == 0) {
-        #pragma unroll
-        for (int mi = 0; mi < 2; ++mi)
-            #pragma unroll
-            for (int j = 0; j < 4; ++j) rowred[mi * 16 + r0 + j][wave] = rs[mi][j];
-    }
-    __syncthreads();
-    float inv[2][4];
-    #pragma unroll
-    for (int mi = 0; mi < 2; ++mi)
-        #pragma unroll
-        for (int j = 0; j < 4; ++j) {
-            const int r = mi * 16 + r0 + j;
-            float s = rowred[r][0] + rowred[r][1] + rowred[r][2] + rowred[r][3];
-            inv[mi][j] = 1.f / fmaxf(sqrtf(s), 1e-12f);
-        }
-    float cs[4];
-    #pragma unroll
-    for (int ni = 0; ni < 4; ++ni) {
-        float s = 0.f;
-        #pragma unroll
-        for (int mi = 0; mi < 2; ++mi)
-            #pragma unroll
-            for (int j = 0; j < 4; ++j) s += acc[mi][ni][j];
-        s += __shfl_xor(s, 16);
-        s += __shfl_xor(s, 32);
-        cs[ni] = s;
-    }
-    if (lane < 16) {
-        #pragma unroll
-        for (int ni = 0; ni < 4; ++ni)
-            psum[(long)p * 256 + wn + ni * 16 + lane] = cs[ni];
-    }
-    #pragma unroll
-    for (int ni = 0; ni < 4; ++ni)
-        #pragma unroll
-        for (int mi = 0; mi < 2; ++mi)
-            #pragma unroll
-            for (int j = 0; j < 4; ++j)
-                n_out[(grow0 + mi * 16 + r0 + j) * 256 + wn + ni * 16 + c0] =
-                    f2b(acc[mi][ni][j] * inv[mi][j]);
 }
 
 __global__ __launch_bounds__(256) void creduce(const float* __restrict__ psum1,
@@ -855,14 +821,12 @@
         fc1T, seq_bf, nullptr, ftsT,
         256, 8192, 128, 128, 128, 8192, 32768, 0, 2097152);
 
-    gcn1qk<<<dim3(16, 16), 256, 0, stream>>>(adj_bf, ftsT, qwT, outT, q_bf, k_bf);
-
-    gemm_norm<<<dim3(1, 16, 16), 256, 0, stream>>>(
-        diff_bf, fts2T, n2_bf, psum2, bias2, prelu2_a, 512, 512, 8192, 262144, 512);
-
-    attmlp<<<dim3(16, 16), 256, 0, stream>>>(
+    gcn1qk<<<dim3(32, 16), 256, 0, stream>>>(adj_bf, ftsT, qwT, outT, q_bf, k_bf);
+
+    attmlp_h2<<<512, 256, 0, stream>>>(
         q_bf, k_bf, adj_bf, drop, outT, vw1T, vw2T, bias1, v_prelu, prelu1_a,
-        n1_bf, psum1, rowpart);
+        n1_bf, psum1, rowpart,
+        diff_bf, fts2T, bias2, prelu2_a, n2_bf, psum2);
 
     creduce<<<32, 256, 0, stream>>>(psum1, psum2, c1n, c2n);
     graphf3<<<1, 256, 0, stream>>>(c1n, c2n, rowpart, out + 67108864, out + 67109120);
```

After: 212.6 us. About the same (+0.0%).
